# Kernel optimization log

Measured on AMD Instinct MI355X. Metric: run time of the kernel, lower is better.

## Reference

```python
import jax, jax.numpy as jnp
import numpy as np

B, S, D_MODEL, N_HEADS, HIDDEN = 4, 2048, 1024, 16, 4096
D_HEAD = D_MODEL // N_HEADS
LN_EPS = 1e-5


def setup_inputs() -> dict:
    key = jax.random.key(0)
    ks = jax.random.split(key, 20)
    s = 0.02
    return {
        "X": jax.random.normal(ks[0], (B, S, D_MODEL), dtype=jnp.float32),
        # attention projections (stored [in, out]; y = x @ W + b)
        "Wq": jax.random.normal(ks[1], (D_MODEL, D_MODEL), dtype=jnp.float32) * s,
        "bq": jnp.zeros((D_MODEL,), jnp.float32),
        "Wk": jax.random.normal(ks[2], (D_MODEL, D_MODEL), dtype=jnp.float32) * s,
        "bk": jnp.zeros((D_MODEL,), jnp.float32),
        "Wv": jax.random.normal(ks[3], (D_MODEL, D_MODEL), dtype=jnp.float32) * s,
        "bv": jnp.zeros((D_MODEL,), jnp.float32),
        "Wo": jax.random.normal(ks[4], (D_MODEL, D_MODEL), dtype=jnp.float32) * s,
        "bo": jnp.zeros((D_MODEL,), jnp.float32),
        # layernorm 1
        "g1": jnp.ones((D_MODEL,), jnp.float32),
        "beta1": jnp.zeros((D_MODEL,), jnp.float32),
        # FFN
        "W1": jax.random.normal(ks[5], (D_MODEL, HIDDEN), dtype=jnp.float32) * s,
        "b1": jnp.zeros((HIDDEN,), jnp.float32),
        "W2": jax.random.normal(ks[6], (HIDDEN, D_MODEL), dtype=jnp.float32) * s,
        "b2": jnp.zeros((D_MODEL,), jnp.float32),
        # layernorm 2
        "g2": jnp.ones((D_MODEL,), jnp.float32),
        "beta2": jnp.zeros((D_MODEL,), jnp.float32),
    }


def _layer_norm(x, gamma, beta):
    mu = jnp.mean(x, axis=-1, keepdims=True)
    var = jnp.mean(jnp.square(x - mu), axis=-1, keepdims=True)
    return (x - mu) * jax.lax.rsqrt(var + LN_EPS) * gamma + beta


def reference(X, Wq, bq, Wk, bk, Wv, bv, Wo, bo, g1, beta1, W1, b1, W2, b2, g2, beta2):
    b, s, d = X.shape
    # multi-head attention (dropout is identity in eval mode)
    q = (X @ Wq + bq).reshape(b, s, N_HEADS, D_HEAD)
    k = (X @ Wk + bk).reshape(b, s, N_HEADS, D_HEAD)
    v = (X @ Wv + bv).reshape(b, s, N_HEADS, D_HEAD)
    scale = 1.0 / np.sqrt(D_HEAD).astype(np.float32)
    scores = jnp.einsum('bqhd,bkhd->bhqk', q, k) * scale
    attn = jax.nn.softmax(scores, axis=-1)
    ctx = jnp.einsum('bhqk,bkhd->bqhd', attn, v).reshape(b, s, d)
    attn_out = ctx @ Wo + bo
    # AddNorm 1
    Y = _layer_norm(X + attn_out, g1, beta1)
    # FFN
    ffn_out = jax.nn.relu(Y @ W1 + b1) @ W2 + b2
    # AddNorm 2
    return _layer_norm(Y + ffn_out, g2, beta2)
```

## Files before the change

### kernel.cpp

```cpp
#include <hip/hip_runtime.h>
#include <stdint.h>

typedef unsigned short u16;
typedef short bf16x8 __attribute__((ext_vector_type(8)));
typedef float f32x4 __attribute__((ext_vector_type(4)));
typedef u16 u16x4 __attribute__((ext_vector_type(4)));
typedef u16 u16x8 __attribute__((ext_vector_type(8)));

#define LOG2E 1.4426950408889634f
#define QSCALE (0.125f * LOG2E)

__device__ __forceinline__ u16 f2bf(float f) {
  union { float f; uint32_t u; } x; x.f = f;
  uint32_t r = x.u + 0x7fffu + ((x.u >> 16) & 1u);
  return (u16)(r >> 16);
}
__device__ __forceinline__ u16 f2bf_ru(float f) {
  union { float f; uint32_t u; } x; x.f = f;
  return (u16)((x.u + 0x8000u) >> 16);
}
__device__ __forceinline__ float bf2f(u16 h) {
  union { uint32_t u; float f; } x; x.u = ((uint32_t)h) << 16;
  return x.f;
}
__device__ __forceinline__ uint32_t cvtpk(float lo, float hi) {
  uint32_t r;
  asm("v_cvt_pk_bf16_f32 %0, %1, %2" : "=v"(r) : "v"(lo), "v"(hi));
  return r;
}
__device__ __forceinline__ int swz3(int row) { return (row ^ (row >> 3)) & 7; }

__device__ __forceinline__ void gload_lds16(const void* g, void* lds) {
  __builtin_amdgcn_global_load_lds(
      (const __attribute__((address_space(1))) void*)g,
      (__attribute__((address_space(3))) void*)lds, 16, 0, 0);
}

__global__ __launch_bounds__(256) void cast_bf16(const float* __restrict__ in,
                                                 u16* __restrict__ out, int n8) {
  int i = blockIdx.x * 256 + threadIdx.x;
  const int stride = gridDim.x * 256;
  for (; i < n8; i += stride) {
    const f32x4* p = (const f32x4*)in + (size_t)i * 2;
    f32x4 a = p[0], b = p[1];
    u16x8 o;
    o[0] = f2bf(a[0]); o[1] = f2bf(a[1]); o[2] = f2bf(a[2]); o[3] = f2bf(a[3]);
    o[4] = f2bf(b[0]); o[5] = f2bf(b[1]); o[6] = f2bf(b[2]); o[7] = f2bf(b[3]);
    ((u16x8*)out)[i] = o;
  }
}

__global__ __launch_bounds__(256) void concat3(const float* __restrict__ a,
                                               const float* __restrict__ b,
                                               const float* __restrict__ c,
                                               float* __restrict__ o) {
  int i = blockIdx.x * 256 + threadIdx.x;
  if (i < 3072)
    o[i] = i < 1024 ? a[i] * QSCALE : (i < 2048 ? b[i - 1024] : c[i - 2048]);
}

__global__ __launch_bounds__(256) void transpose_cast(const float* __restrict__ in,
                                                      u16* __restrict__ out, int R, int C,
                                                      float scale) {
  __shared__ float tile[32][33];
  const int bc = blockIdx.x * 32, br = blockIdx.y * 32;
  const int tx = threadIdx.x & 31, ty = threadIdx.x >> 5;
#pragma unroll
  for (int i = 0; i < 32; i += 8)
    tile[ty + i][tx] = in[(size_t)(br + ty + i) * C + bc + tx];
  __syncthreads();
#pragma unroll
  for (int i = 0; i < 32; i += 8)
    out[(size_t)(bc + ty + i) * R + br + tx] = f2bf(tile[tx][ty + i] * scale);
}

__global__ __launch_bounds__(256) void vtrans(const u16* __restrict__ QKV,
                                              u16* __restrict__ Vtg) {
  __shared__ u16 tl[64][65];
  const int t = threadIdx.x;
  const int sblk = blockIdx.x, h = blockIdx.y, b = blockIdx.z;
  const int s0 = sblk * 64;
  const size_t ibase = ((size_t)b * 2048) * 3072 + 2048 + h * 64;
#pragma unroll
  for (int i = 0; i < 2; i++) {
    const int idx = i * 256 + t;
    const int sl = idx >> 3, d0 = (idx & 7) * 8;
    bf16x8 v = *(const bf16x8*)&QKV[ibase + (size_t)(s0 + sl) * 3072 + d0];
#pragma unroll
    for (int e = 0; e < 8; e++) tl[d0 + e][sl] = (u16)v[e];
  }
  __syncthreads();
  const size_t ob = ((size_t)(b * 16 + h) * 64) * 2048;
#pragma unroll
  for (int i = 0; i < 2; i++) {
    const int idx = i * 256 + t;
    const int r = idx >> 3, c0 = (idx & 7) * 8;
    u16x8 o;
#pragma unroll
    for (int e = 0; e < 8; e++) o[e] = tl[r][c0 + e];
    *(u16x8*)&Vtg[ob + (size_t)r * 2048 + s0 + c0] = o;
  }
}

template <int RELU>
__global__ __launch_bounds__(256) void gemm_bt(const u16* __restrict__ A,
                                               const u16* __restrict__ BT,
                                               const float* __restrict__ bias,
                                               u16* __restrict__ Cb,
                                               int M, int N, int K) {
  constexpr int BM = 128, BN = 128, BK = 64;
  __shared__ u16 As[BM * BK];
  __shared__ u16 Bs[BN * BK];
  const int t = threadIdx.x;
  const int w = t >> 6, lane = t & 63;
  const int la = lane & 15, lb = lane >> 4;
  const int wr = w >> 1, wc = w & 1;
  const int m0 = blockIdx.y * BM, n0 = blockIdx.x * BN;

  f32x4 acc[4][4];
#pragma unroll
  for (int i = 0; i < 4; i++)
#pragma unroll
    for (int j = 0; j < 4; j++) acc[i][j] = (f32x4){0.f, 0.f, 0.f, 0.f};

  for (int kt = 0; kt < K; kt += BK) {
#pragma unroll
    for (int i = 0; i < 4; i++) {
      const int s = i * 256 + t;
      const int row = s >> 3, col = (s & 7) * 8;
      gload_lds16(A + (size_t)(m0 + row) * K + kt + col, &As[(i * 256 + w * 64) * 8]);
      gload_lds16(BT + (size_t)(n0 + row) * K + kt + col, &Bs[(i * 256 + w * 64) * 8]);
    }
    __syncthreads();
#pragma unroll
    for (int ks = 0; ks < 2; ks++) {
      bf16x8 af[4], bfr[4];
#pragma unroll
      for (int i = 0; i < 4; i++)
        af[i] = *(const bf16x8*)&As[(wr * 64 + i * 16 + la) * BK + ks * 32 + lb * 8];
#pragma unroll
      for (int j = 0; j < 4; j++)
        bfr[j] = *(const bf16x8*)&Bs[(wc * 64 + j * 16 + la) * BK + ks * 32 + lb * 8];
#pragma unroll
      for (int i = 0; i < 4; i++)
#pragma unroll
        for (int j = 0; j < 4; j++)
          acc[i][j] = __builtin_amdgcn_mfma_f32_16x16x32_bf16(af[i], bfr[j], acc[i][j], 0, 0, 0);
    }
    __syncthreads();
  }
#pragma unroll
  for (int i = 0; i < 4; i++) {
    const int r = m0 + wr * 64 + i * 16 + lb * 4;
#pragma unroll
    for (int j = 0; j < 4; j++) {
      const int c = n0 + wc * 64 + j * 16 + la;
      const float bv = bias[c];
#pragma unroll
      for (int rr = 0; rr < 4; rr++) {
        float v = acc[i][j][rr] + bv;
        if (RELU) v = fmaxf(v, 0.f);
        Cb[(size_t)(r + rr) * N + c] = f2bf(v);
      }
    }
  }
}

template <int RELU>
__global__ __launch_bounds__(512, 2) void gemm8p(const u16* __restrict__ A,
                                                 const u16* __restrict__ BT,
                                                 const float* __restrict__ bias,
                                                 u16* __restrict__ Cb,
                                                 int M, int N, int K, int nbx) {
  __shared__ u16 As[2][256 * 64];
  __shared__ u16 Bs[2][256 * 64];
  const int t = threadIdx.x;
  const int w = t >> 6, lane = t & 63;
  const int la = lane & 15, lb = lane >> 4;
  const int wr = w >> 2, wc = w & 3;
  int bid = (int)blockIdx.x;
  const int cpx = (int)gridDim.x >> 3;
  bid = (bid & 7) * cpx + (bid >> 3);
  const int m0 = (bid / nbx) * 256, n0 = (bid % nbx) * 256;
  const int NT = K >> 6;
  const int row64 = t >> 3;
  const int colp = ((t & 7) ^ swz3(row64)) << 3;

#define STG_A(buf, tile, q) \
  gload_lds16(A + (size_t)(m0 + (q)*64 + row64) * K + ((tile) << 6) + colp, \
              &As[buf][(q)*4096 + w * 512])
#define STG_B(buf, tile, q) \
  gload_lds16(BT + (size_t)(n0 + (q)*64 + row64) * K + ((tile) << 6) + colp, \
              &Bs[buf][(q)*4096 + w * 512])
#define LDA(dst, mf, ks) { const int r_ = wr * 128 + (mf)*16 + la; \
  dst = *(const bf16x8*)&As[cur][r_ * 64 + (((((ks) << 2) + lb) ^ swz3(r_)) << 3)]; }
#define LDB(dst, nf, ks) { const int r_ = wc * 64 + (nf)*16 + la; \
  dst = *(const bf16x8*)&Bs[cur][r_ * 64 + (((((ks) << 2) + lb) ^ swz3(r_)) << 3)]; }
#define MFMA16(mh, nh) \
  __builtin_amdgcn_s_setprio(1); \
  _Pragma("unroll") for (int ks = 0; ks < 2; ks++) \
  _Pragma("unroll") for (int i = 0; i < 4; i++) \
  _Pragma("unroll") for (int j = 0; j < 2; j++) \
    acc[(mh)*4 + i][(nh)*2 + j] = __builtin_amdgcn_mfma_f32_16x16x32_bf16( \
        af[i][ks], bfr[j][ks], acc[(mh)*4 + i][(nh)*2 + j], 0, 0, 0); \
  __builtin_amdgcn_s_setprio(0);
#define BAR1() __builtin_amdgcn_s_barrier(); \
  asm volatile("s_waitcnt lgkmcnt(0)" ::: "memory"); \
  __builtin_amdgcn_sched_barrier(0)

  f32x4 acc[8][4];
#pragma unroll
  for (int i = 0; i < 8; i++)
#pragma unroll
    for (int j = 0; j < 4; j++) acc[i][j] = (f32x4){0.f, 0.f, 0.f, 0.f};

  STG_A(0, 0, 0); STG_A(0, 0, 2);
  STG_B(0, 0, 0); STG_B(0, 0, 1); STG_B(0, 0, 2); STG_B(0, 0, 3);
  STG_A(0, 0, 1); STG_A(0, 0, 3);
  asm volatile("s_waitcnt vmcnt(2)" ::: "memory");
  __builtin_amdgcn_s_barrier();

  for (int tile = 0; tile < NT; ++tile) {
    const int cur = tile & 1, nxt = cur ^ 1;
    const bool hn = (tile + 1) < NT;
    bf16x8 af[4][2], bfr[2][2];
#pragma unroll
    for (int i = 0; i < 4; i++) { LDA(af[i][0], i, 0); LDA(af[i][1], i, 1); }
#pragma unroll
    for (int j = 0; j < 2; j++) { LDB(bfr[j][0], j, 0); LDB(bfr[j][1], j, 1); }
    if (hn) { STG_A(nxt, tile + 1, 0); STG_A(nxt, tile + 1, 2); }
    BAR1();
    MFMA16(0, 0);
    __builtin_amdgcn_s_barrier();
#pragma unroll
    for (int j = 0; j < 2; j++) { LDB(bfr[j][0], 2 + j, 0); LDB(bfr[j][1], 2 + j, 1); }
    if (hn) { STG_B(nxt, tile + 1, 0); STG_B(nxt, tile + 1, 1); }
    BAR1();
    MFMA16(0, 1);
    if (hn) { asm volatile("s_waitcnt vmcnt(4)" ::: "memory"); }
    else    { asm volatile("s_waitcnt vmcnt(0)" ::: "memory"); }
    __builtin_amdgcn_s_barrier();
#pragma unroll
    for (int i = 0; i < 4; i++) { LDA(af[i][0], 4 + i, 0); LDA(af[i][1], 4 + i, 1); }
#pragma unroll
    for (int j = 0; j < 2; j++) { LDB(bfr[j][0], j, 0); LDB(bfr[j][1], j, 1); }
    if (hn) { STG_B(nxt, tile + 1, 2); STG_B(nxt, tile + 1, 3); }
    BAR1();
    MFMA16(1, 0);
    __builtin_amdgcn_s_barrier();
#pragma unroll
    for (int j = 0; j < 2; j++) { LDB(bfr[j][0], 2 + j, 0); LDB(bfr[j][1], 2 + j, 1); }
    if (hn) { STG_A(nxt, tile + 1, 1); STG_A(nxt, tile + 1, 3); }
    BAR1();
    MFMA16(1, 1);
    if (hn) { asm volatile("s_waitcnt vmcnt(2)" ::: "memory"); }
    __builtin_amdgcn_s_barrier();
  }
#undef STG_A
#undef STG_B
#undef LDA
#undef LDB
#undef MFMA16
#undef BAR1

#pragma unroll
  for (int mf = 0; mf < 8; mf++) {
    const int r = m0 + wr * 128 + mf * 16 + lb * 4;
#pragma unroll
    for (int nf = 0; nf < 4; nf++) {
      const int c = n0 + wc * 64 + nf * 16 + la;
      const float bv = bias[c];
#pragma unroll
      for (int rr = 0; rr < 4; rr++) {
        float v = acc[mf][nf][rr] + bv;
        if (RELU) v = fmaxf(v, 0.f);
        Cb[(size_t)(r + rr) * N + c] = f2bf(v);
      }
    }
  }
}

__global__ __launch_bounds__(256) void attn_fwd(const u16* __restrict__ Qg,
                                                const u16* __restrict__ Kg,
                                                const u16* __restrict__ Vtg,
                                                u16* __restrict__ Og, int LDM) {
  constexpr int S = 2048, DMO = 1024;
  __shared__ u16 Ks[2][128 * 64];
  __shared__ u16 Vt[2][64 * 128];
  const int t = threadIdx.x, w = t >> 6, lane = t & 63;
  const int la = lane & 15, lb = lane >> 4;
  const int qb = blockIdx.x, h = blockIdx.y, b = blockIdx.z;
  const size_t base = ((size_t)b * S) * LDM + h * 64;
  const size_t vbase = ((size_t)(b * 16 + h) * 64) * 2048;
  const size_t obase = ((size_t)b * S) * DMO + h * 64;
  const int qrow0 = qb * 128 + w * 32;
  const int sl0 = la + 32 * (lb & 1), sl1 = sl0 + 16;
  const int jsel = lb >> 1;

#define ATT_STAGE(buf, kt_) { \
  _Pragma("unroll") for (int i = 0; i < 4; i++) { \
    const int s = i * 256 + t; const int r = s >> 3; const int cg = s & 7; \
    gload_lds16(Kg + base + (size_t)((kt_) + r) * LDM + ((cg ^ swz3(r)) << 3), \
                &Ks[buf][s * 8]); } \
  _Pragma("unroll") for (int i = 0; i < 4; i++) { \
    const int s = i * 256 + t; const int r = s >> 4; const int cg = s & 15; \
    gload_lds16(Vtg + vbase + (size_t)r * 2048 + (kt_) + ((cg ^ swz3(r)) << 3), \
                &Vt[buf][s * 8]); } }

  bf16x8 qf[2][2];
#pragma unroll
  for (int rf = 0; rf < 2; rf++)
#pragma unroll
    for (int ks = 0; ks < 2; ks++)
      qf[rf][ks] = *(const bf16x8*)&Qg[base + (size_t)(qrow0 + rf * 16 + la) * LDM + ks * 32 + lb * 8];

  f32x4 accO[2][4];
  float m[2], l[2];
#pragma unroll
  for (int i = 0; i < 2; i++) {
    m[i] = -1e30f; l[i] = 0.f;
#pragma unroll
    for (int j = 0; j < 4; j++) accO[i][j] = (f32x4){0.f, 0.f, 0.f, 0.f};
  }

  ATT_STAGE(0, 0);
  asm volatile("s_waitcnt vmcnt(0)" ::: "memory");
  __builtin_amdgcn_s_barrier();

  for (int kt2 = 0; kt2 < S / 128; ++kt2) {
    const int cur = kt2 & 1;
    if (kt2 + 1 < S / 128) ATT_STAGE(cur ^ 1, (kt2 + 1) * 128);

#pragma unroll
    for (int sub = 0; sub < 2; ++sub) {
      f32x4 st[4][2];
#pragma unroll
      for (int j = 0; j < 4; j++)
#pragma unroll
        for (int rf = 0; rf < 2; rf++) st[j][rf] = (f32x4){0.f, 0.f, 0.f, 0.f};
      __builtin_amdgcn_s_setprio(1);
#pragma unroll
      for (int ks = 0; ks < 2; ks++) {
        bf16x8 kf[4];
#pragma unroll
        for (int j = 0; j < 4; j++) {
          const int r = sub * 64 + j * 16 + la;
          kf[j] = *(const bf16x8*)&Ks[cur][r * 64 + ((((ks << 2) + lb) ^ swz3(r)) << 3)];
        }
#pragma unroll
        for (int j = 0; j < 4; j++)
#pragma unroll
          for (int rf = 0; rf < 2; rf++)
            st[j][rf] = __builtin_amdgcn_mfma_f32_16x16x32_bf16(kf[j], qf[rf][ks], st[j][rf], 0, 0, 0);
      }
      __builtin_amdgcn_s_setprio(0);

      bf16x8 pf[2][2];
#pragma unroll
      for (int rf = 0; rf < 2; rf++) {
        float rm = st[0][rf][0];
#pragma unroll
        for (int j = 0; j < 4; j++)
#pragma unroll
          for (int rr = 0; rr < 4; rr++) rm = fmaxf(rm, st[j][rf][rr]);
        if (__any(rm > m[rf] + 8.0f)) {
          rm = fmaxf(rm, __shfl_xor(rm, 16, 64));
          rm = fmaxf(rm, __shfl_xor(rm, 32, 64));
          const float mN = fmaxf(m[rf], rm);
          const float al = exp2f(m[rf] - mN);
          m[rf] = mN;
          l[rf] *= al;
#pragma unroll
          for (int rr = 0; rr < 4; rr++) {
            const float alr = __shfl(al, (lb << 2) + rr, 64);
#pragma unroll
            for (int cf = 0; cf < 4; cf++) accO[rf][cf][rr] *= alr;
          }
        }
        uint32_t wl[4], wh[4];
#pragma unroll
        for (int j = 0; j < 4; j++) {
          float p0 = exp2f(st[j][rf][0] - m[rf]);
          float p1 = exp2f(st[j][rf][1] - m[rf]);
          float p2 = exp2f(st[j][rf][2] - m[rf]);
          float p3 = exp2f(st[j][rf][3] - m[rf]);
          l[rf] += (p0 + p1) + (p2 + p3);
          wl[j] = cvtpk(p0, p1);
          wh[j] = cvtpk(p2, p3);
        }
#pragma unroll
        for (int ks = 0; ks < 2; ks++) {
          const int j0 = 2 * ks, j1 = 2 * ks + 1;
          uint32_t a0 = __shfl(wl[j0], sl0, 64), a1 = __shfl(wh[j0], sl0, 64);
          uint32_t a2 = __shfl(wl[j0], sl1, 64), a3 = __shfl(wh[j0], sl1, 64);
          uint32_t b0 = __shfl(wl[j1], sl0, 64), b1 = __shfl(wh[j1], sl0, 64);
          uint32_t b2 = __shfl(wl[j1], sl1, 64), b3 = __shfl(wh[j1], sl1, 64);
          union { uint32_t u[4]; bf16x8 v; } pk;
          pk.u[0] = jsel ? b0 : a0;
          pk.u[1] = jsel ? b1 : a1;
          pk.u[2] = jsel ? b2 : a2;
          pk.u[3] = jsel ? b3 : a3;
          pf[rf][ks] = pk.v;
        }
      }

      __builtin_amdgcn_s_setprio(1);
#pragma unroll
      for (int ks = 0; ks < 2; ks++) {
        bf16x8 vf[4];
#pragma unroll
        for (int cf = 0; cf < 4; cf++) {
          const int dr = cf * 16 + la;
          const int g = sub * 8 + ks * 4 + lb;
          vf[cf] = *(const bf16x8*)&Vt[cur][dr * 128 + ((g ^ swz3(dr)) << 3)];
        }
#pragma unroll
        for (int rf = 0; rf < 2; rf++)
#pragma unroll
          for (int cf = 0; cf < 4; cf++)
            accO[rf][cf] = __builtin_amdgcn_mfma_f32_16x16x32_bf16(pf[rf][ks], vf[cf], accO[rf][cf], 0, 0, 0);
      }
      __builtin_amdgcn_s_setprio(0);
    }

    asm volatile("s_waitcnt vmcnt(0)" ::: "memory");
    __builtin_amdgcn_s_barrier();
  }
#undef ATT_STAGE

#pragma unroll
  for (int rf = 0; rf < 2; rf++) {
    float l2 = l[rf];
    l2 += __shfl_xor(l2, 16, 64);
    l2 += __shfl_xor(l2, 32, 64);
    const float inv = 1.0f / l2;
#pragma unroll
    for (int rr = 0; rr < 4; rr++) {
      const float invr = __shfl(inv, (lb << 2) + rr, 64);
      const int r = qrow0 + rf * 16 + lb * 4 + rr;
#pragma unroll
      for (int cf = 0; cf < 4; cf++)
        Og[obase + (size_t)r * DMO + cf * 16 + la] = f2bf_ru(accO[rf][cf][rr] * invr);
    }
  }
}

template <int AF32, int OUTF32>
__global__ __launch_bounds__(256) void add_ln(const void* __restrict__ Ap,
                                              const u16* __restrict__ Bb,
                                              const float* __restrict__ g,
                                              const float* __restrict__ be,
                                              void* __restrict__ Yp) {
  constexpr int D = 1024;
  const int row = blockIdx.x, t = threadIdx.x;
  f32x4 a;
  if (AF32) {
    a = ((const f32x4*)((const float*)Ap + (size_t)row * D))[t];
  } else {
    u16x4 av = ((const u16x4*)((const u16*)Ap + (size_t)row * D))[t];
#pragma unroll
    for (int i = 0; i < 4; i++) a[i] = bf2f(av[i]);
  }
  u16x4 bv16 = ((const u16x4*)(Bb + (size_t)row * D))[t];
  f32x4 x;
#pragma unroll
  for (int i = 0; i < 4; i++) x[i] = a[i] + bf2f(bv16[i]);
  float s1 = x[0] + x[1] + x[2] + x[3];
  float s2 = x[0] * x[0] + x[1] * x[1] + x[2] * x[2] + x[3] * x[3];
#pragma unroll
  for (int off = 32; off > 0; off >>= 1) {
    s1 += __shfl_down(s1, off, 64);
    s2 += __shfl_down(s2, off, 64);
  }
  __shared__ float sm[8];
  const int w = t >> 6, lane = t & 63;
  if (lane == 0) { sm[w] = s1; sm[4 + w] = s2; }
  __syncthreads();
  s1 = sm[0] + sm[1] + sm[2] + sm[3];
  s2 = sm[4] + sm[5] + sm[6] + sm[7];
  const float mean = s1 * (1.0f / D);
  const float var = s2 * (1.0f / D) - mean * mean;
  const float rstd = rsqrtf(var + 1e-5f);
  const f32x4 gv = ((const f32x4*)g)[t];
  const f32x4 bv = ((const f32x4*)be)[t];
  f32x4 y;
#pragma unroll
  for (int i = 0; i < 4; i++) y[i] = (x[i] - mean) * rstd * gv[i] + bv[i];
  if (OUTF32) {
    ((f32x4*)((float*)Yp + (size_t)row * D))[t] = y;
  } else {
    u16x4 o;
#pragma unroll
    for (int i = 0; i < 4; i++) o[i] = f2bf(y[i]);
    ((u16x4*)((u16*)Yp + (size_t)row * D))[t] = o;
  }
}

extern "C" void kernel_launch(void* const* d_in, const int* in_sizes, int n_in,
                              void* d_out, int out_size, void* d_ws, size_t ws_size,
                              hipStream_t stream) {
  const float* X   = (const float*)d_in[0];
  const float* Wq  = (const float*)d_in[1];
  const float* bq  = (const float*)d_in[2];
  const float* Wk  = (const float*)d_in[3];
  const float* bk  = (const float*)d_in[4];
  const float* Wv  = (const float*)d_in[5];
  const float* bv  = (const float*)d_in[6];
  const float* Wo  = (const float*)d_in[7];
  const float* bo  = (const float*)d_in[8];
  const float* g1  = (const float*)d_in[9];
  const float* be1 = (const float*)d_in[10];
  const float* W1  = (const float*)d_in[11];
  const float* b1  = (const float*)d_in[12];
  const float* W2  = (const float*)d_in[13];
  const float* b2  = (const float*)d_in[14];
  const float* g2  = (const float*)d_in[15];
  const float* be2 = (const float*)d_in[16];

  const size_t MB = 1ull << 20;
  char* wsb = (char*)d_ws;
  u16*   WqkvT = (u16*)(wsb + 0 * MB);
  u16*   WoT   = (u16*)(wsb + 6 * MB);
  u16*   W1T   = (u16*)(wsb + 8 * MB);
  u16*   W2T   = (u16*)(wsb + 16 * MB);
  u16*   Xb    = (u16*)(wsb + 24 * MB);
  u16*   Ab    = (u16*)(wsb + 24 * MB);
  u16*   Fb    = (u16*)(wsb + 24 * MB);
  u16*   QKVb  = (u16*)(wsb + 40 * MB);
  u16*   Hb    = (u16*)(wsb + 40 * MB);
  float* bqkv  = (float*)(wsb + 88 * MB);
  u16*   Cx    = (u16*)(wsb + 88 * MB);
  u16*   Vt_g  = (u16*)(wsb + 104 * MB);
  u16*   Yb    = (u16*)(wsb + 104 * MB);
  (void)ws_size; (void)in_sizes; (void)n_in; (void)out_size;

  cast_bf16<<<2048, 256, 0, stream>>>(X, Xb, 8192 * 1024 / 8);
  concat3<<<12, 256, 0, stream>>>(bq, bk, bv, bqkv);
  transpose_cast<<<dim3(32, 32), 256, 0, stream>>>(Wq, WqkvT, 1024, 1024, QSCALE);
  transpose_cast<<<dim3(32, 32), 256, 0, stream>>>(Wk, WqkvT + 1024 * 1024, 1024, 1024, 1.0f);
  transpose_cast<<<dim3(32, 32), 256, 0, stream>>>(Wv, WqkvT + 2 * 1024 * 1024, 1024, 1024, 1.0f);
  transpose_cast<<<dim3(32, 32), 256, 0, stream>>>(Wo, WoT, 1024, 1024, 1.0f);
  transpose_cast<<<dim3(128, 32), 256, 0, stream>>>(W1, W1T, 1024, 4096, 1.0f);
  transpose_cast<<<dim3(32, 128), 256, 0, stream>>>(W2, W2T, 4096, 1024, 1.0f);

  gemm8p<0><<<32 * 12, 512, 0, stream>>>(Xb, WqkvT, bqkv, QKVb, 8192, 3072, 1024, 12);

  vtrans<<<dim3(32, 16, 4), 256, 0, stream>>>(QKVb, Vt_g);
  attn_fwd<<<dim3(16, 16, 4), 256, 0, stream>>>(QKVb, QKVb + 1024, Vt_g, Cx, 3072);

  gemm_bt<0><<<dim3(8, 64), 256, 0, stream>>>(Cx, WoT, bo, Ab, 8192, 1024, 1024);
  add_ln<1, 0><<<8192, 256, 0, stream>>>(X, Ab, g1, be1, Yb);
  gemm8p<1><<<32 * 16, 512, 0, stream>>>(Yb, W1T, b1, Hb, 8192, 4096, 1024, 16);
  gemm_bt<0><<<dim3(8, 64), 256, 0, stream>>>(Hb, W2T, b2, Fb, 8192, 1024, 4096);
  add_ln<0, 1><<<8192, 256, 0, stream>>>(Yb, Fb, g2, be2, d_out);
}
```

Measured before the change: 502.8 us.

## Reuse B fragments across GEMM halves and shrink attention KV tile to 64

In gemm8p, the B fragments loaded for the first M half are kept in two register sets (b0, b1) and reused for the second M half, which removes two rounds of LDS reads per K tile at the cost of more VGPRs. In attn_fwd, the K/V staging tile drops from 128 to 64 keys with one compute pass per tile, halving LDS use and possibly raising occupancy, but doubling the number of loop iterations and barriers. Grid sizes written as products are replaced by their literal values, which changes nothing.

```diff
diff --git a/kernel.cpp b/kernel.cpp
--- a/kernel.cpp
+++ b/kernel.cpp
@@ -196,13 +196,13 @@
   dst = *(const bf16x8*)&As[cur][r_ * 64 + (((((ks) << 2) + lb) ^ swz3(r_)) << 3)]; }
 #define LDB(dst, nf, ks) { const int r_ = wc * 64 + (nf)*16 + la; \
   dst = *(const bf16x8*)&Bs[cur][r_ * 64 + (((((ks) << 2) + lb) ^ swz3(r_)) << 3)]; }
-#define MFMA16(mh, nh) \
+#define MFMA16(mh, nh, barr) \
   __builtin_amdgcn_s_setprio(1); \
   _Pragma("unroll") for (int ks = 0; ks < 2; ks++) \
   _Pragma("unroll") for (int i = 0; i < 4; i++) \
   _Pragma("unroll") for (int j = 0; j < 2; j++) \
     acc[(mh)*4 + i][(nh)*2 + j] = __builtin_amdgcn_mfma_f32_16x16x32_bf16( \
-        af[i][ks], bfr[j][ks], acc[(mh)*4 + i][(nh)*2 + j], 0, 0, 0); \
+        af[i][ks], barr[j][ks], acc[(mh)*4 + i][(nh)*2 + j], 0, 0, 0); \
   __builtin_amdgcn_s_setprio(0);
 #define BAR1() __builtin_amdgcn_s_barrier(); \
   asm volatile("s_waitcnt lgkmcnt(0)" ::: "memory"); \
@@ -223,36 +223,32 @@
   for (int tile = 0; tile < NT; ++tile) {
     const int cur = tile & 1, nxt = cur ^ 1;
     const bool hn = (tile + 1) < NT;
-    bf16x8 af[4][2], bfr[2][2];
+    bf16x8 af[4][2], b0[2][2], b1[2][2];
 #pragma unroll
     for (int i = 0; i < 4; i++) { LDA(af[i][0], i, 0); LDA(af[i][1], i, 1); }
 #pragma unroll
-    for (int j = 0; j < 2; j++) { LDB(bfr[j][0], j, 0); LDB(bfr[j][1], j, 1); }
+    for (int j = 0; j < 2; j++) { LDB(b0[j][0], j, 0); LDB(b0[j][1], j, 1); }
     if (hn) { STG_A(nxt, tile + 1, 0); STG_A(nxt, tile + 1, 2); }
     BAR1();
-    MFMA16(0, 0);
+    MFMA16(0, 0, b0);
     __builtin_amdgcn_s_barrier();
 #pragma unroll
-    for (int j = 0; j < 2; j++) { LDB(bfr[j][0], 2 + j, 0); LDB(bfr[j][1], 2 + j, 1); }
+    for (int j = 0; j < 2; j++) { LDB(b1[j][0], 2 + j, 0); LDB(b1[j][1], 2 + j, 1); }
     if (hn) { STG_B(nxt, tile + 1, 0); STG_B(nxt, tile + 1, 1); }
     BAR1();
-    MFMA16(0, 1);
+    MFMA16(0, 1, b1);
     if (hn) { asm volatile("s_waitcnt vmcnt(4)" ::: "memory"); }
     else    { asm volatile("s_waitcnt vmcnt(0)" ::: "memory"); }
     __builtin_amdgcn_s_barrier();
 #pragma unroll
     for (int i = 0; i < 4; i++) { LDA(af[i][0], 4 + i, 0); LDA(af[i][1], 4 + i, 1); }
-#pragma unroll
-    for (int j = 0; j < 2; j++) { LDB(bfr[j][0], j, 0); LDB(bfr[j][1], j, 1); }
     if (hn) { STG_B(nxt, tile + 1, 2); STG_B(nxt, tile + 1, 3); }
     BAR1();
-    MFMA16(1, 0);
+    MFMA16(1, 0, b0);
     __builtin_amdgcn_s_barrier();
-#pragma unroll
-    for (int j = 0; j < 2; j++) { LDB(bfr[j][0], 2 + j, 0); LDB(bfr[j][1], 2 + j, 1); }
     if (hn) { STG_A(nxt, tile + 1, 1); STG_A(nxt, tile + 1, 3); }
     BAR1();
-    MFMA16(1, 1);
+    MFMA16(1, 1, b1);
     if (hn) { asm volatile("s_waitcnt vmcnt(2)" ::: "memory"); }
     __builtin_amdgcn_s_barrier();
   }
@@ -284,9 +280,9 @@
                                                 const u16* __restrict__ Kg,
                                                 const u16* __restrict__ Vtg,
                                                 u16* __restrict__ Og, int LDM) {
-  constexpr int S = 2048, DMO = 1024;
-  __shared__ u16 Ks[2][128 * 64];
-  __shared__ u16 Vt[2][64 * 128];
+  constexpr int S = 2048, DMO = 1024, NT = S / 64;
+  __shared__ u16 Ks[2][64 * 64];
+  __shared__ u16 Vt[2][64 * 64];
   const int t = threadIdx.x, w = t >> 6, lane = t & 63;
   const int la = lane & 15, lb = lane >> 4;
   const int qb = blockIdx.x, h = blockIdx.y, b = blockIdx.z;
@@ -298,12 +294,12 @@
   const int jsel = lb >> 1;
 
 #define ATT_STAGE(buf, kt_) { \
-  _Pragma("unroll") for (int i = 0; i < 4; i++) { \
+  _Pragma("unroll") for (int i = 0; i < 2; i++) { \
     const int s = i * 256 + t; const int r = s >> 3; const int cg = s & 7; \
     gload_lds16(Kg + base + (size_t)((kt_) + r) * LDM + ((cg ^ swz3(r)) << 3), \
                 &Ks[buf][s * 8]); } \
-  _Pragma("unroll") for (int i = 0; i < 4; i++) { \
-    const int s = i * 256 + t; const int r = s >> 4; const int cg = s & 15; \
+  _Pragma("unroll") for (int i = 0; i < 2; i++) { \
+    const int s = i * 256 + t; const int r = s >> 3; const int cg = s & 7; \
     gload_lds16(Vtg + vbase + (size_t)r * 2048 + (kt_) + ((cg ^ swz3(r)) << 3), \
                 &Vt[buf][s * 8]); } }
 
@@ -327,101 +323,97 @@
   asm volatile("s_waitcnt vmcnt(0)" ::: "memory");
   __builtin_amdgcn_s_barrier();
 
-  for (int kt2 = 0; kt2 < S / 128; ++kt2) {
-    const int cur = kt2 & 1;
-    if (kt2 + 1 < S / 128) ATT_STAGE(cur ^ 1, (kt2 + 1) * 128);
-
-#pragma unroll
-    for (int sub = 0; sub < 2; ++sub) {
-      f32x4 st[4][2];
+  for (int kt = 0; kt < NT; ++kt) {
+    const int cur = kt & 1;
+    if (kt + 1 < NT) ATT_STAGE(cur ^ 1, (kt + 1) * 64);
+
+    f32x4 st[4][2];
+#pragma unroll
+    for (int j = 0; j < 4; j++)
+#pragma unroll
+      for (int rf = 0; rf < 2; rf++) st[j][rf] = (f32x4){0.f, 0.f, 0.f, 0.f};
+    __builtin_amdgcn_s_setprio(1);
+#pragma unroll
+    for (int ks = 0; ks < 2; ks++) {
+      bf16x8 kf[4];
+#pragma unroll
+      for (int j = 0; j < 4; j++) {
+        const int r = j * 16 + la;
+        kf[j] = *(const bf16x8*)&Ks[cur][r * 64 + ((((ks << 2) + lb) ^ swz3(r)) << 3)];
+      }
 #pragma unroll
       for (int j = 0; j < 4; j++)
 #pragma unroll
-        for (int rf = 0; rf < 2; rf++) st[j][rf] = (f32x4){0.f, 0.f, 0.f, 0.f};
-      __builtin_amdgcn_s_setprio(1);
+        for (int rf = 0; rf < 2; rf++)
+          st[j][rf] = __builtin_amdgcn_mfma_f32_16x16x32_bf16(kf[j], qf[rf][ks], st[j][rf], 0, 0, 0);
+    }
+    __builtin_amdgcn_s_setprio(0);
+
+    bf16x8 pf[2][2];
+#pragma unroll
+    for (int rf = 0; rf < 2; rf++) {
+      float rm = st[0][rf][0];
+#pragma unroll
+      for (int j = 0; j < 4; j++)
+#pragma unroll
+        for (int rr = 0; rr < 4; rr++) rm = fmaxf(rm, st[j][rf][rr]);
+      if (__any(rm > m[rf] + 8.0f)) {
+        rm = fmaxf(rm, __shfl_xor(rm, 16, 64));
+        rm = fmaxf(rm, __shfl_xor(rm, 32, 64));
+        const float mN = fmaxf(m[rf], rm);
+        const float al = exp2f(m[rf] - mN);
+        m[rf] = mN;
+        l[rf] *= al;
+#pragma unroll
+        for (int rr = 0; rr < 4; rr++) {
+          const float alr = __shfl(al, (lb << 2) + rr, 64);
+#pragma unroll
+          for (int cf = 0; cf < 4; cf++) accO[rf][cf][rr] *= alr;
+        }
+      }
+      uint32_t wl[4], wh[4];
+#pragma unroll
+      for (int j = 0; j < 4; j++) {
+        float p0 = exp2f(st[j][rf][0] - m[rf]);
+        float p1 = exp2f(st[j][rf][1] - m[rf]);
+        float p2 = exp2f(st[j][rf][2] - m[rf]);
+        float p3 = exp2f(st[j][rf][3] - m[rf]);
+        l[rf] += (p0 + p1) + (p2 + p3);
+        wl[j] = cvtpk(p0, p1);
+        wh[j] = cvtpk(p2, p3);
+      }
 #pragma unroll
       for (int ks = 0; ks < 2; ks++) {
-        bf16x8 kf[4];
-#pragma unroll
-        for (int j = 0; j < 4; j++) {
-          const int r = sub * 64 + j * 16 + la;
-          kf[j] = *(const bf16x8*)&Ks[cur][r * 64 + ((((ks << 2) + lb) ^ swz3(r)) << 3)];
-        }
-#pragma unroll
-        for (int j = 0; j < 4; j++)
-#pragma unroll
-          for (int rf = 0; rf < 2; rf++)
-            st[j][rf] = __builtin_amdgcn_mfma_f32_16x16x32_bf16(kf[j], qf[rf][ks], st[j][rf], 0, 0, 0);
-      }
-      __builtin_amdgcn_s_setprio(0);
-
-      bf16x8 pf[2][2];
-#pragma unroll
-      for (int rf = 0; rf < 2; rf++) {
-        float rm = st[0][rf][0];
-#pragma unroll
-        for (int j = 0; j < 4; j++)
-#pragma unroll
-          for (int rr = 0; rr < 4; rr++) rm = fmaxf(rm, st[j][rf][rr]);
-        if (__any(rm > m[rf] + 8.0f)) {
-          rm = fmaxf(rm, __shfl_xor(rm, 16, 64));
-          rm = fmaxf(rm, __shfl_xor(rm, 32, 64));
-          const float mN = fmaxf(m[rf], rm);
-          const float al = exp2f(m[rf] - mN);
-          m[rf] = mN;
-          l[rf] *= al;
-#pragma unroll
-          for (int rr = 0; rr < 4; rr++) {
-            const float alr = __shfl(al, (lb << 2) + rr, 64);
-#pragma unroll
-            for (int cf = 0; cf < 4; cf++) accO[rf][cf][rr] *= alr;
-          }
-        }
-        uint32_t wl[4], wh[4];
-#pragma unroll
-        for (int j = 0; j < 4; j++) {
-          float p0 = exp2f(st[j][rf][0] - m[rf]);
-          float p1 = exp2f(st[j][rf][1] - m[rf]);
-          float p2 = exp2f(st[j][rf][2] - m[rf]);
-          float p3 = exp2f(st[j][rf][3] - m[rf]);
-          l[rf] += (p0 + p1) + (p2 + p3);
-          wl[j] = cvtpk(p0, p1);
-          wh[j] = cvtpk(p2, p3);
-        }
-#pragma unroll
-        for (int ks = 0; ks < 2; ks++) {
-          const int j0 = 2 * ks, j1 = 2 * ks + 1;
-          uint32_t a0 = __shfl(wl[j0], sl0, 64), a1 = __shfl(wh[j0], sl0, 64);
-          uint32_t a2 = __shfl(wl[j0], sl1, 64), a3 = __shfl(wh[j0], sl1, 64);
-          uint32_t b0 = __shfl(wl[j1], sl0, 64), b1 = __shfl(wh[j1], sl0, 64);
-          uint32_t b2 = __shfl(wl[j1], sl1, 64), b3 = __shfl(wh[j1], sl1, 64);
-          union { uint32_t u[4]; bf16x8 v; } pk;
-          pk.u[0] = jsel ? b0 : a0;
-          pk.u[1] = jsel ? b1 : a1;
-          pk.u[2] = jsel ? b2 : a2;
-          pk.u[3] = jsel ? b3 : a3;
-          pf[rf][ks] = pk.v;
-        }
-      }
-
-      __builtin_amdgcn_s_setprio(1);
-#pragma unroll
-      for (int ks = 0; ks < 2; ks++) {
-        bf16x8 vf[4];
-#pragma unroll
-        for (int cf = 0; cf < 4; cf++) {
-          const int dr = cf * 16 + la;
-          const int g = sub * 8 + ks * 4 + lb;
-          vf[cf] = *(const bf16x8*)&Vt[cur][dr * 128 + ((g ^ swz3(dr)) << 3)];
-        }
-#pragma unroll
-        for (int rf = 0; rf < 2; rf++)
-#pragma unroll
-          for (int cf = 0; cf < 4; cf++)
-            accO[rf][cf] = __builtin_amdgcn_mfma_f32_16x16x32_bf16(pf[rf][ks], vf[cf], accO[rf][cf], 0, 0, 0);
-      }
-      __builtin_amdgcn_s_setprio(0);
-    }
+        const int j0 = 2 * ks, j1 = 2 * ks + 1;
+        uint32_t a0 = __shfl(wl[j0], sl0, 64), a1 = __shfl(wh[j0], sl0, 64);
+        uint32_t a2 = __shfl(wl[j0], sl1, 64), a3 = __shfl(wh[j0], sl1, 64);
+        uint32_t b0 = __shfl(wl[j1], sl0, 64), b1 = __shfl(wh[j1], sl0, 64);
+        uint32_t b2 = __shfl(wl[j1], sl1, 64), b3 = __shfl(wh[j1], sl1, 64);
+        union { uint32_t u[4]; bf16x8 v; } pk;
+        pk.u[0] = jsel ? b0 : a0;
+        pk.u[1] = jsel ? b1 : a1;
+        pk.u[2] = jsel ? b2 : a2;
+        pk.u[3] = jsel ? b3 : a3;
+        pf[rf][ks] = pk.v;
+      }
+    }
+
+    __builtin_amdgcn_s_setprio(1);
+#pragma unroll
+    for (int ks = 0; ks < 2; ks++) {
+      bf16x8 vf[4];
+#pragma unroll
+      for (int cf = 0; cf < 4; cf++) {
+        const int dr = cf * 16 + la;
+        vf[cf] = *(const bf16x8*)&Vt[cur][dr * 64 + ((((ks << 2) + lb) ^ swz3(dr)) << 3)];
+      }
+#pragma unroll
+      for (int rf = 0; rf < 2; rf++)
+#pragma unroll
+        for (int cf = 0; cf < 4; cf++)
+          accO[rf][cf] = __builtin_amdgcn_mfma_f32_16x16x32_bf16(pf[rf][ks], vf[cf], accO[rf][cf], 0, 0, 0);
+    }
+    __builtin_amdgcn_s_setprio(0);
 
     asm volatile("s_waitcnt vmcnt(0)" ::: "memory");
     __builtin_amdgcn_s_barrier();
@@ -543,14 +535,14 @@
   transpose_cast<<<dim3(128, 32), 256, 0, stream>>>(W1, W1T, 1024, 4096, 1.0f);
   transpose_cast<<<dim3(32, 128), 256, 0, stream>>>(W2, W2T, 4096, 1024, 1.0f);
 
-  gemm8p<0><<<32 * 12, 512, 0, stream>>>(Xb, WqkvT, bqkv, QKVb, 8192, 3072, 1024, 12);
+  gemm8p<0><<<384, 512, 0, stream>>>(Xb, WqkvT, bqkv, QKVb, 8192, 3072, 1024, 12);
 
   vtrans<<<dim3(32, 16, 4), 256, 0, stream>>>(QKVb, Vt_g);
   attn_fwd<<<dim3(16, 16, 4), 256, 0, stream>>>(QKVb, QKVb + 1024, Vt_g, Cx, 3072);
 
   gemm_bt<0><<<dim3(8, 64), 256, 0, stream>>>(Cx, WoT, bo, Ab, 8192, 1024, 1024);
   add_ln<1, 0><<<8192, 256, 0, stream>>>(X, Ab, g1, be1, Yb);
-  gemm8p<1><<<32 * 16, 512, 0, stream>>>(Yb, W1T, b1, Hb, 8192, 4096, 1024, 16);
+  gemm8p<1><<<512, 512, 0, stream>>>(Yb, W1T, b1, Hb, 8192, 4096, 1024, 16);
   gemm_bt<0><<<dim3(8, 64), 256, 0, stream>>>(Hb, W2T, b2, Fb, 8192, 1024, 4096);
   add_ln<0, 1><<<8192, 256, 0, stream>>>(Yb, Fb, g2, be2, d_out);
 }
```

Measured after the change: 489.3 us. -2.7%, faster.
